# Kernel optimization log

Hardware: AMD Instinct MI355X
Metric: run time of the kernel (lower is better)

The kernel has to match this reference:

```python
import jax, jax.numpy as jnp
import numpy as np

B, C, H, W = 8, 512, 96, 96

def setup_inputs() -> dict:
    key = jax.random.key(0)
    k1, k2, k3, k4, k5 = jax.random.split(key, 5)
    s = 0.02
    return {
        "x": jax.random.normal(k1, (B, C, H, W), dtype=jnp.float32),
        "w_qkv": jax.random.normal(k2, (3 * C, C), dtype=jnp.float32) * s,
        "b_qkv": jax.random.normal(k3, (3 * C,), dtype=jnp.float32) * s,
        "w_proj": jax.random.normal(k4, (C, C), dtype=jnp.float32) * s,
        "b_proj": jax.random.normal(k5, (C,), dtype=jnp.float32) * s,
    }

def reference(x, w_qkv, b_qkv, w_proj, b_proj):
    b, c, h, w = x.shape
    n = h * w
    # 1x1 conv == pointwise linear over channels
    qkv = jnp.einsum('bchw,oc->bohw', x, w_qkv) + b_qkv[None, :, None, None]
    qkv = qkv.reshape(b, 3, c, n)
    q, k, v = qkv[:, 0], qkv[:, 1], qkv[:, 2]  # each [B, C, N]
    # channel attention: scores are [B, C, C]
    scale = 1.0 / (c ** 0.5)
    attn = jax.nn.softmax(jnp.einsum('bcn,bdn->bcd', q, k) * scale, axis=-1)
    out = jnp.einsum('bcd,bdn->bcn', attn, v).reshape(b, c, h, w)
    out = jnp.einsum('bchw,oc->bohw', out, w_proj) + b_proj[None, :, None, None]
    return out
```

## Files before the change

### kernel.cpp

```cpp
#include <hip/hip_runtime.h>

typedef unsigned short u16;
typedef unsigned long long u64;
typedef __bf16 bf16x8 __attribute__((ext_vector_type(8)));
typedef u16 us8 __attribute__((ext_vector_type(8)));
typedef u16 us4 __attribute__((ext_vector_type(4)));
typedef float floatx4 __attribute__((ext_vector_type(4)));
typedef float f32x4 __attribute__((ext_vector_type(4)));

__device__ inline float b2f(u16 u) {
  union { unsigned u; float f; } x; x.u = ((unsigned)u) << 16; return x.f;
}
__device__ inline u16 f2b(float f) {
  union { float f; unsigned u; } x; x.f = f;
  unsigned r = x.u + 0x7fffu + ((x.u >> 16) & 1u);
  return (u16)(r >> 16);
}

__global__ __launch_bounds__(256)
void detect_dtype(const u16* __restrict__ x, int* __restrict__ flag, int force) {
  __shared__ float sm[4];
  const int t = threadIdx.x;
  float m = 0.f;
  for (int i = t; i < 4096; i += 256) {
    float v = fabsf(b2f(x[i]));
    if (v > m) m = v;
  }
#pragma unroll
  for (int o = 32; o; o >>= 1) m = fmaxf(m, __shfl_xor(m, o, 64));
  if ((t & 63) == 0) sm[t >> 6] = m;
  __syncthreads();
  if (t == 0) {
    float mm = fmaxf(fmaxf(sm[0], sm[1]), fmaxf(sm[2], sm[3]));
    *flag = (force >= 0) ? force : (mm > 1000.0f ? 1 : 0);
  }
}

__global__ __launch_bounds__(256)
void convert_bf16(const void* __restrict__ in, u16* __restrict__ out, long n,
                  const int* __restrict__ flag) {
  const long i = (blockIdx.x * 256L + threadIdx.x) * 8;
  if (i >= n) return;
  if (*flag) {
    const float* p = (const float*)in + i;
    f32x4 a = ((const f32x4*)p)[0];
    f32x4 b = ((const f32x4*)p)[1];
    us8 o;
#pragma unroll
    for (int j = 0; j < 4; j++) { o[j] = f2b(a[j]); o[j + 4] = f2b(b[j]); }
    *(us8*)(out + i) = o;
  } else {
    *(us8*)(out + i) = *((const us8*)in + (i >> 3));
  }
}

template <typename OutT>
__global__ __launch_bounds__(256)
void gemm_nt(const u16* __restrict__ A, long sA, int lda,
             const u16* __restrict__ B, long sB, int ldb,
             OutT* __restrict__ D, long sD, int ldd, int K) {
  __shared__ __align__(16) u16 As[128 * 32];
  __shared__ __align__(16) u16 Bs[128 * 32];
  const int bz = blockIdx.z;
  const u16* Ab = A + (long)bz * sA;
  const u16* Bb = B + (long)bz * sB;
  OutT* Db = D + (long)bz * sD;
  const int tid  = threadIdx.x;
  const int lane = tid & 63;
  const int wave = tid >> 6;
  const int wm = (wave >> 1) * 64, wn = (wave & 1) * 64;
  const int m0 = blockIdx.y * 128, n0 = blockIdx.x * 128;
  const int srow = tid >> 2;
  const int ss   = tid & 3;
  const int sw   = (ss ^ ((srow >> 1) & 3)) * 8;
  const int lr = lane & 15;
  const int rsw = (((lane >> 4) ^ ((lr >> 1) & 3)) * 8);

  floatx4 acc[4][4];
#pragma unroll
  for (int i = 0; i < 4; i++)
#pragma unroll
    for (int j = 0; j < 4; j++) acc[i][j] = (floatx4){0.f, 0.f, 0.f, 0.f};

  for (int k0 = 0; k0 < K; k0 += 32) {
    __syncthreads();
    *(bf16x8*)&As[srow * 32 + sw] =
        *(const bf16x8*)&Ab[(long)(m0 + srow) * lda + k0 + ss * 8];
    *(bf16x8*)&As[(srow + 64) * 32 + sw] =
        *(const bf16x8*)&Ab[(long)(m0 + srow + 64) * lda + k0 + ss * 8];
    *(bf16x8*)&Bs[srow * 32 + sw] =
        *(const bf16x8*)&Bb[(long)(n0 + srow) * ldb + k0 + ss * 8];
    *(bf16x8*)&Bs[(srow + 64) * 32 + sw] =
        *(const bf16x8*)&Bb[(long)(n0 + srow + 64) * ldb + k0 + ss * 8];
    __syncthreads();
    bf16x8 af[4], bfr[4];
#pragma unroll
    for (int i = 0; i < 4; i++)
      af[i] = *(bf16x8*)&As[(wm + i * 16 + lr) * 32 + rsw];
#pragma unroll
    for (int i = 0; i < 4; i++)
      bfr[i] = *(bf16x8*)&Bs[(wn + i * 16 + lr) * 32 + rsw];
#pragma unroll
    for (int mi = 0; mi < 4; mi++)
#pragma unroll
      for (int ni = 0; ni < 4; ni++)
        acc[mi][ni] = __builtin_amdgcn_mfma_f32_16x16x32_bf16(
            af[mi], bfr[ni], acc[mi][ni], 0, 0, 0);
  }

  const int lc  = lane & 15;
  const int lr4 = (lane >> 4) * 4;
#pragma unroll
  for (int mi = 0; mi < 4; mi++) {
#pragma unroll
    for (int r = 0; r < 4; r++) {
      int gm = m0 + wm + mi * 16 + lr4 + r;
#pragma unroll
      for (int ni = 0; ni < 4; ni++) {
        int gn = n0 + wn + ni * 16 + lc;
        float v = acc[mi][ni][r];
        if constexpr (sizeof(OutT) == 4) Db[(long)gm * ldd + gn] = v;
        else                             Db[(long)gm * ldd + gn] = f2b(v);
      }
    }
  }
}

__device__ inline void tile_decode(int t, int& by, int& bx) {
  by = (int)((sqrtf((float)(8 * t + 1)) - 1.0f) * 0.5f);
  bx = t - (by * (by + 1)) / 2;
}

__global__ __launch_bounds__(256)
void gemm_xxt_splitk(const u16* __restrict__ X, float* __restrict__ P) {
  __shared__ __align__(16) u16 As[128 * 32];
  __shared__ __align__(16) u16 Bs[128 * 32];
  const int t  = blockIdx.x;
  const int bz = blockIdx.z >> 3;
  const int sp = blockIdx.z & 7;
  int by, bx;
  tile_decode(t, by, bx);
  const int m0 = by * 128, n0 = bx * 128;
  const u16* Xb = X + (long)bz * 512 * 9216;
  const int tid  = threadIdx.x;
  const int lane = tid & 63;
  const int wave = tid >> 6;
  const int wm = (wave >> 1) * 64, wn = (wave & 1) * 64;
  const int srow = tid >> 2;
  const int ss   = tid & 3;
  const int sw   = (ss ^ ((srow >> 1) & 3)) * 8;
  const int lr = lane & 15;
  const int rsw = (((lane >> 4) ^ ((lr >> 1) & 3)) * 8);

  floatx4 acc[4][4];
#pragma unroll
  for (int i = 0; i < 4; i++)
#pragma unroll
    for (int j = 0; j < 4; j++) acc[i][j] = (floatx4){0.f, 0.f, 0.f, 0.f};

  const int k0beg = sp * 1152;
  for (int k0 = k0beg; k0 < k0beg + 1152; k0 += 32) {
    __syncthreads();
    *(bf16x8*)&As[srow * 32 + sw] =
        *(const bf16x8*)&Xb[(long)(m0 + srow) * 9216 + k0 + ss * 8];
    *(bf16x8*)&As[(srow + 64) * 32 + sw] =
        *(const bf16x8*)&Xb[(long)(m0 + srow + 64) * 9216 + k0 + ss * 8];
    *(bf16x8*)&Bs[srow * 32 + sw] =
        *(const bf16x8*)&Xb[(long)(n0 + srow) * 9216 + k0 + ss * 8];
    *(bf16x8*)&Bs[(srow + 64) * 32 + sw] =
        *(const bf16x8*)&Xb[(long)(n0 + srow + 64) * 9216 + k0 + ss * 8];
    __syncthreads();
    bf16x8 af[4], bfr[4];
#pragma unroll
    for (int i = 0; i < 4; i++)
      af[i] = *(bf16x8*)&As[(wm + i * 16 + lr) * 32 + rsw];
#pragma unroll
    for (int i = 0; i < 4; i++)
      bfr[i] = *(bf16x8*)&Bs[(wn + i * 16 + lr) * 32 + rsw];
#pragma unroll
    for (int mi = 0; mi < 4; mi++)
#pragma unroll
      for (int ni = 0; ni < 4; ni++)
        acc[mi][ni] = __builtin_amdgcn_mfma_f32_16x16x32_bf16(
            af[mi], bfr[ni], acc[mi][ni], 0, 0, 0);
  }

  float* Pb = P + ((long)(sp * 8 + bz) * 10 + t) * 16384;
  const int lc  = lane & 15;
  const int lr4 = (lane >> 4) * 4;
#pragma unroll
  for (int mi = 0; mi < 4; mi++)
#pragma unroll
    for (int r = 0; r < 4; r++) {
      int gm = wm + mi * 16 + lr4 + r;
#pragma unroll
      for (int ni = 0; ni < 4; ni++)
        Pb[gm * 128 + wn + ni * 16 + lc] = acc[mi][ni][r];
    }
}

__global__ __launch_bounds__(256)
void reduce_xxt(const float* __restrict__ P, u16* __restrict__ G) {
  __shared__ u16 tl[128][130];
  const int t = blockIdx.x, bz = blockIdx.y;
  int by, bx;
  tile_decode(t, by, bx);
  const int m0 = by * 128, n0 = bx * 128;
  u16* Gb = G + (long)bz * 512 * 512;
  for (int e = threadIdx.x; e < 4096; e += 256) {
    const int idx = e * 4;
    const int m = idx >> 7, n = idx & 127;
    f32x4 s = {0.f, 0.f, 0.f, 0.f};
#pragma unroll
    for (int sp = 0; sp < 8; sp++) {
      f32x4 v = *(const f32x4*)&P[(((long)sp * 8 + bz) * 10 + t) * 16384 + idx];
      s.x += v.x; s.y += v.y; s.z += v.z; s.w += v.w;
    }
    us4 o = {f2b(s.x), f2b(s.y), f2b(s.z), f2b(s.w)};
    *(us4*)&Gb[(long)(m0 + m) * 512 + n0 + n] = o;
    tl[m][n] = o[0]; tl[m][n + 1] = o[1]; tl[m][n + 2] = o[2]; tl[m][n + 3] = o[3];
  }
  if (m0 == n0) return;
  __syncthreads();
  for (int e = threadIdx.x; e < 4096; e += 256) {
    const int idx = e * 4;
    const int nr = idx >> 7, mc = idx & 127;
    us4 o = {tl[mc][nr], tl[mc + 1][nr], tl[mc + 2][nr], tl[mc + 3][nr]};
    *(us4*)&Gb[(long)(n0 + nr) * 512 + m0 + mc] = o;
  }
}

__global__ __launch_bounds__(256)
void gemm_nn_out(const u16* __restrict__ A, const u16* __restrict__ B,
                 const float* __restrict__ bias, void* __restrict__ Dout,
                 const int* __restrict__ flag) {
  __shared__ __align__(16)  u16 As[128 * 32];
  __shared__ __align__(128) u16 Bs[32 * 128];
  const int f = *flag;
  const int bz = blockIdx.z;
  const u16* Ab = A + (long)bz * 512 * 512;
  const u16* Bb = B + (long)bz * 512 * 9216;
  const float* cb = bias + bz * 512;
  const int tid  = threadIdx.x;
  const int lane = tid & 63;
  const int wave = tid >> 6;
  const int wm = (wave >> 1) * 64, wn = (wave & 1) * 64;
  const int m0 = blockIdx.y * 128, n0 = blockIdx.x * 128;
  const int srow = tid >> 2;
  const int ss   = tid & 3;
  const int sw   = (ss ^ ((srow >> 1) & 3)) * 8;
  const int kk  = tid >> 3;
  const int nbw = tid & 7;
  const int lr = lane & 15;
  const int rsw = (((lane >> 4) ^ ((lr >> 1) & 3)) * 8);
  const int stO = (nbw * 8 + (kk >> 2)) * 64 + (kk & 3) * 16;
  const unsigned bsBase = (unsigned)(size_t)(&Bs[0]);
  const unsigned trA = bsBase + (unsigned)((wn >> 4) * 1024 +
                       (lane >> 4) * 256 + (lane & 15) * 8);

  floatx4 acc[4][4];
#pragma unroll
  for (int i = 0; i < 4; i++)
#pragma unroll
    for (int j = 0; j < 4; j++) acc[i][j] = (floatx4){0.f, 0.f, 0.f, 0.f};

  for (int k0 = 0; k0 < 512; k0 += 32) {
    __syncthreads();
    *(bf16x8*)&As[srow * 32 + sw] =
        *(const bf16x8*)&Ab[(long)(m0 + srow) * 512 + k0 + ss * 8];
    *(bf16x8*)&As[(srow + 64) * 32 + sw] =
        *(const bf16x8*)&Ab[(long)(m0 + srow + 64) * 512 + k0 + ss * 8];
    us8 v0 = *(const us8*)&Bb[(long)(k0 + kk) * 9216 + n0 + nbw * 16];
    us8 v1 = *(const us8*)&Bb[(long)(k0 + kk) * 9216 + n0 + nbw * 16 + 8];
    *(us8*)&Bs[stO]     = v0;
    *(us8*)&Bs[stO + 8] = v1;
    __syncthreads();
    bf16x8 af[4];
#pragma unroll
    for (int i = 0; i < 4; i++)
      af[i] = *(bf16x8*)&As[(wm + i * 16 + lr) * 32 + rsw];
    u64 blo[4], bhi[4];
#pragma unroll
    for (int ni = 0; ni < 4; ni++) {
      unsigned a = trA + ni * 1024;
      asm volatile("ds_read_b64_tr_b16 %0, %1" : "=v"(blo[ni]) : "v"(a));
      asm volatile("ds_read_b64_tr_b16 %0, %1 offset:128" : "=v"(bhi[ni]) : "v"(a));
    }
    asm volatile("s_waitcnt lgkmcnt(0)" ::: "memory");
    __builtin_amdgcn_sched_barrier(0);
    bf16x8 bfr[4];
#pragma unroll
    for (int ni = 0; ni < 4; ni++) {
      union { u64 q[2]; bf16x8 v; } u;
      u.q[0] = blo[ni]; u.q[1] = bhi[ni];
      bfr[ni] = u.v;
    }
#pragma unroll
    for (int mi = 0; mi < 4; mi++)
#pragma unroll
      for (int ni = 0; ni < 4; ni++)
        acc[mi][ni] = __builtin_amdgcn_mfma_f32_16x16x32_bf16(
            af[mi], bfr[ni], acc[mi][ni], 0, 0, 0);
  }

  const int lc  = lane & 15;
  const int lr4 = (lane >> 4) * 4;
  if (f) {
    float* Db = (float*)Dout + (long)bz * 512 * 9216;
#pragma unroll
    for (int mi = 0; mi < 4; mi++)
#pragma unroll
      for (int r = 0; r < 4; r++) {
        int gm = m0 + wm + mi * 16 + lr4 + r;
        float bv = cb[gm];
#pragma unroll
        for (int ni = 0; ni < 4; ni++)
          Db[(long)gm * 9216 + n0 + wn + ni * 16 + lc] = acc[mi][ni][r] + bv;
      }
  } else {
    u16* Db = (u16*)Dout + (long)bz * 512 * 9216;
#pragma unroll
    for (int mi = 0; mi < 4; mi++)
#pragma unroll
      for (int r = 0; r < 4; r++) {
        int gm = m0 + wm + mi * 16 + lr4 + r;
        float bv = cb[gm];
#pragma unroll
        for (int ni = 0; ni < 4; ni++)
          Db[(long)gm * 9216 + n0 + wn + ni * 16 + lc] = f2b(acc[mi][ni][r] + bv);
      }
  }
}

__global__ __launch_bounds__(256)
void rowsum(const u16* __restrict__ x, float* __restrict__ r) {
  const int row  = blockIdx.x * 4 + (threadIdx.x >> 6);
  const int lane = threadIdx.x & 63;
  const u16* p = x + (long)row * 9216;
  float s = 0.f;
#pragma unroll
  for (int t = 0; t < 18; t++) {
    us8 v = *(const us8*)&p[t * 512 + lane * 8];
#pragma unroll
    for (int e = 0; e < 8; e++) s += b2f(v[e]);
  }
#pragma unroll
  for (int o = 32; o; o >>= 1) s += __shfl_xor(s, o, 64);
  if (lane == 0) r[row] = s;
}

__global__ __launch_bounds__(256)
void matvec_uw(const u16* __restrict__ w_qkv, const float* __restrict__ r,
               float* __restrict__ u, float* __restrict__ w) {
  const int g = blockIdx.x * 256 + threadIdx.x;
  const int b = g >> 10;
  const int s = (g >> 9) & 1;
  const int i = g & 511;
  const u16* Wrow = w_qkv + (long)(s * 512 + i) * 512;
  const float* rb = r + b * 512;
  float acc = 0.f;
  for (int c = 0; c < 512; c++) acc += b2f(Wrow[c]) * rb[c];
  (s ? w : u)[b * 512 + i] = acc;
}

__global__ __launch_bounds__(256)
void cvec(const u16* __restrict__ w_proj, const float* __restrict__ y,
          const u16* __restrict__ b_proj, float* __restrict__ cv) {
  const int g = blockIdx.x * 256 + threadIdx.x;
  const int b = g >> 9;
  const int o = g & 511;
  const u16* Wrow = w_proj + (long)o * 512;
  const float* yb = y + b * 512;
  float acc = 0.f;
  for (int i = 0; i < 512; i++) acc += b2f(Wrow[i]) * yb[i];
  cv[b * 512 + o] = acc + b2f(b_proj[o]);
}

__global__ __launch_bounds__(256)
void softmax_rank1(const float* __restrict__ Score, const float* __restrict__ u,
                   const float* __restrict__ w, const u16* __restrict__ b_qkv,
                   u16* __restrict__ PT, float* __restrict__ y) {
  const int row  = blockIdx.x * 4 + (threadIdx.x >> 6);
  const int lane = threadIdx.x & 63;
  const int b = row >> 9, i = row & 511;
  const float scale = 0.04419417382415922f;
  const float* srow = Score + (long)row * 512;
  const float* wb = w + b * 512;
  const float bq_i = b2f(b_qkv[i]);
  const float uu = u[row] + 9216.0f * bq_i;
  float vals[8];
  float mx = -1e30f;
#pragma unroll
  for (int t = 0; t < 8; t++) {
    int j = lane + t * 64;
    float s = srow[j] + uu * b2f(b_qkv[512 + j]) + bq_i * wb[j];
    vals[t] = scale * s;
    mx = fmaxf(mx, vals[t]);
  }
#pragma unroll
  for (int o = 32; o; o >>= 1) mx = fmaxf(mx, __shfl_xor(mx, o, 64));
  float sum = 0.f, ys = 0.f;
#pragma unroll
  for (int t = 0; t < 8; t++) {
    int j = lane + t * 64;
    vals[t] = __expf(vals[t] - mx);
    sum += vals[t];
    ys += vals[t] * b2f(b_qkv[1024 + j]);
  }
#pragma unroll
  for (int o = 32; o; o >>= 1) sum += __shfl_xor(sum, o, 64);
#pragma unroll
  for (int o = 32; o; o >>= 1) ys += __shfl_xor(ys, o, 64);
  const float inv = 1.0f / sum;
#pragma unroll
  for (int t = 0; t < 8; t++) {
    int j = lane + t * 64;
    PT[(long)b * 512 * 512 + (long)j * 512 + i] = f2b(vals[t] * inv);
  }
  if (lane == 0) y[row] = ys * inv;
}

__global__ __launch_bounds__(256)
void transpose512(const u16* __restrict__ in, u16* __restrict__ out) {
  __shared__ u16 tile[32][33];
  const int c0 = blockIdx.x * 32, r0 = blockIdx.y * 32;
  const int tx = threadIdx.x, ty = threadIdx.y;
#pragma unroll
  for (int i = 0; i < 32; i += 8)
    tile[ty + i][tx] = in[(long)(r0 + ty + i) * 512 + c0 + tx];
  __syncthreads();
#pragma unroll
  for (int i = 0; i < 32; i += 8)
    out[(long)(c0 + ty + i) * 512 + r0 + tx] = tile[tx][ty + i];
}

extern "C" void kernel_launch(void* const* d_in, const int* in_sizes, int n_in,
                              void* d_out, int out_size, void* d_ws, size_t ws_size,
                              hipStream_t stream) {
  const long CN = 512L * 9216;
  const long SQ = 512L * 512;

  char* ws = (char*)d_ws;
  int*   flag  = (int*)ws;                      ws += 16;
  u16*   Gb    = (u16*)ws;                      ws += 8 * SQ * 2;
  u16*   T1    = (u16*)ws;                      ws += 8 * SQ * 2;
  u16*   PT    = (u16*)ws;                      ws += 8 * SQ * 2;
  u16*   T3    = (u16*)ws;                      ws += 8 * SQ * 2;
  u16*   Mm    = (u16*)ws;                      ws += 8 * SQ * 2;
  float* Score = (float*)ws;                    ws += 8 * SQ * 4;
  u16*   WvT   = (u16*)ws;                      ws += SQ * 2;
  float* r     = (float*)ws;                    ws += 8 * 512 * 4;
  float* u     = (float*)ws;                    ws += 8 * 512 * 4;
  float* w     = (float*)ws;                    ws += 8 * 512 * 4;
  float* y     = (float*)ws;                    ws += 8 * 512 * 4;
  float* cv    = (float*)ws;                    ws += 8 * 512 * 4;
  u16* xc      = (u16*)ws;                      ws += 8 * CN * 2;
  u16* wqkv_c  = (u16*)ws;                      ws += 1536L * 512 * 2;
  u16* bqkv_c  = (u16*)ws;                      ws += 1536L * 2;
  u16* wproj_c = (u16*)ws;                      ws += 512L * 512 * 2;
  u16* bproj_c = (u16*)ws;                      ws += 512L * 2;

  char* mark1 = ws;
  float* Psk  = (float*)ws;                     ws += 8L * 8 * 10 * 16384 * 4;

  const bool full  = ((size_t)(mark1 - (char*)d_ws) <= ws_size);
  const bool full2 = ((size_t)(ws    - (char*)d_ws) <= ws_size);

  if (full) {
    detect_dtype<<<1, 256, 0, stream>>>((const u16*)d_in[0], flag, -1);
    convert_bf16<<<18432, 256, 0, stream>>>(d_in[0], xc,      8 * CN,      flag);
    convert_bf16<<<384,   256, 0, stream>>>(d_in[1], wqkv_c,  1536L * 512, flag);
    convert_bf16<<<1,     256, 0, stream>>>(d_in[2], bqkv_c,  1536,        flag);
    convert_bf16<<<128,   256, 0, stream>>>(d_in[3], wproj_c, 512L * 512,  flag);
    convert_bf16<<<1,     256, 0, stream>>>(d_in[4], bproj_c, 512,         flag);
  } else {
    detect_dtype<<<1, 256, 0, stream>>>((const u16*)d_in[0], flag, 0);
    xc      = (u16*)d_in[0];
    wqkv_c  = (u16*)d_in[1];
    bqkv_c  = (u16*)d_in[2];
    wproj_c = (u16*)d_in[3];
    bproj_c = (u16*)d_in[4];
  }

  const u16* Wq = wqkv_c;
  const u16* Wk = wqkv_c + 512 * 512;
  const u16* Wv = wqkv_c + 1024 * 512;

  if (full2) {
    gemm_xxt_splitk<<<dim3(10, 1, 64), 256, 0, stream>>>(xc, Psk);
    reduce_xxt<<<dim3(10, 8), 256, 0, stream>>>(Psk, Gb);
  } else {
    gemm_nt<u16><<<dim3(4, 4, 8), 256, 0, stream>>>(
        xc, CN, 9216, xc, CN, 9216, Gb, SQ, 512, 9216);
  }
  rowsum<<<1024, 256, 0, stream>>>(xc, r);
  matvec_uw<<<32, 256, 0, stream>>>(wqkv_c, r, u, w);
  gemm_nt<u16><<<dim3(4, 4, 8), 256, 0, stream>>>(
      Wq, 0, 512, Gb, SQ, 512, T1, SQ, 512, 512);
  gemm_nt<float><<<dim3(4, 4, 8), 256, 0, stream>>>(
      T1, SQ, 512, Wk, 0, 512, Score, SQ, 512, 512);
  softmax_rank1<<<1024, 256, 0, stream>>>(Score, u, w, bqkv_c, PT, y);
  transpose512<<<dim3(16, 16), dim3(32, 8), 0, stream>>>(Wv, WvT);
  gemm_nt<u16><<<dim3(4, 4, 8), 256, 0, stream>>>(
      wproj_c, 0, 512, PT, SQ, 512, T3, SQ, 512, 512);
  gemm_nt<u16><<<dim3(4, 4, 8), 256, 0, stream>>>(
      T3, SQ, 512, WvT, 0, 512, Mm, SQ, 512, 512);
  cvec<<<16, 256, 0, stream>>>(wproj_c, y, bproj_c, cv);
  gemm_nn_out<<<dim3(72, 4, 8), 256, 0, stream>>>(Mm, xc, cv, d_out, flag);
}
```

Baseline: 572.6 us.

## Use direct global-to-LDS loads in GEMMs and shrink small GEMM tiles

Replaces register-staged global loads and LDS stores with global_load_lds direct-to-LDS transfers in gemm_nt, the split-K XX^T GEMM and the output GEMM. The per-wave LDS destinations are arranged so the existing swizzle and transposed read pattern still hold. The 512x512 batched GEMMs also drop from 128x128 to 64x64 tiles, launched on an 8x8x8 grid, to put more blocks on the device. This aims to cut VGPR traffic and instruction count for staging and to improve occupancy on the small GEMMs, at the cost of less reuse per tile.

```diff
diff --git a/kernel.cpp b/kernel.cpp
--- a/kernel.cpp
+++ b/kernel.cpp
@@ -15,6 +15,12 @@
   union { float f; unsigned u; } x; x.f = f;
   unsigned r = x.u + 0x7fffu + ((x.u >> 16) & 1u);
   return (u16)(r >> 16);
+}
+
+__device__ __forceinline__ void gl_lds16(const u16* g, void* l) {
+  __builtin_amdgcn_global_load_lds(
+      (const __attribute__((address_space(1))) void*)g,
+      (__attribute__((address_space(3))) void*)l, 16, 0, 0);
 }
 
 __global__ __launch_bounds__(256)
@@ -59,8 +65,8 @@
 void gemm_nt(const u16* __restrict__ A, long sA, int lda,
              const u16* __restrict__ B, long sB, int ldb,
              OutT* __restrict__ D, long sD, int ldd, int K) {
-  __shared__ __align__(16) u16 As[128 * 32];
-  __shared__ __align__(16) u16 Bs[128 * 32];
+  __shared__ __align__(16) u16 As[64 * 32];
+  __shared__ __align__(16) u16 Bs[64 * 32];
   const int bz = blockIdx.z;
   const u16* Ab = A + (long)bz * sA;
   const u16* Bb = B + (long)bz * sB;
@@ -68,42 +74,38 @@
   const int tid  = threadIdx.x;
   const int lane = tid & 63;
   const int wave = tid >> 6;
-  const int wm = (wave >> 1) * 64, wn = (wave & 1) * 64;
-  const int m0 = blockIdx.y * 128, n0 = blockIdx.x * 128;
+  const int wm = (wave >> 1) * 32, wn = (wave & 1) * 32;
+  const int m0 = blockIdx.y * 64, n0 = blockIdx.x * 64;
   const int srow = tid >> 2;
   const int ss   = tid & 3;
-  const int sw   = (ss ^ ((srow >> 1) & 3)) * 8;
+  const int sco  = (ss ^ ((srow >> 1) & 3)) * 8;
   const int lr = lane & 15;
   const int rsw = (((lane >> 4) ^ ((lr >> 1) & 3)) * 8);
-
-  floatx4 acc[4][4];
-#pragma unroll
-  for (int i = 0; i < 4; i++)
-#pragma unroll
-    for (int j = 0; j < 4; j++) acc[i][j] = (floatx4){0.f, 0.f, 0.f, 0.f};
+  char* asb = (char*)As + wave * 1024;
+  char* bsb = (char*)Bs + wave * 1024;
+
+  floatx4 acc[2][2];
+#pragma unroll
+  for (int i = 0; i < 2; i++)
+#pragma unroll
+    for (int j = 0; j < 2; j++) acc[i][j] = (floatx4){0.f, 0.f, 0.f, 0.f};
 
   for (int k0 = 0; k0 < K; k0 += 32) {
     __syncthreads();
-    *(bf16x8*)&As[srow * 32 + sw] =
-        *(const bf16x8*)&Ab[(long)(m0 + srow) * lda + k0 + ss * 8];
-    *(bf16x8*)&As[(srow + 64) * 32 + sw] =
-        *(const bf16x8*)&Ab[(long)(m0 + srow + 64) * lda + k0 + ss * 8];
-    *(bf16x8*)&Bs[srow * 32 + sw] =
-        *(const bf16x8*)&Bb[(long)(n0 + srow) * ldb + k0 + ss * 8];
-    *(bf16x8*)&Bs[(srow + 64) * 32 + sw] =
-        *(const bf16x8*)&Bb[(long)(n0 + srow + 64) * ldb + k0 + ss * 8];
+    gl_lds16(&Ab[(long)(m0 + srow) * lda + k0 + sco], asb);
+    gl_lds16(&Bb[(long)(n0 + srow) * ldb + k0 + sco], bsb);
     __syncthreads();
-    bf16x8 af[4], bfr[4];
-#pragma unroll
-    for (int i = 0; i < 4; i++)
+    bf16x8 af[2], bfr[2];
+#pragma unroll
+    for (int i = 0; i < 2; i++)
       af[i] = *(bf16x8*)&As[(wm + i * 16 + lr) * 32 + rsw];
 #pragma unroll
-    for (int i = 0; i < 4; i++)
+    for (int i = 0; i < 2; i++)
       bfr[i] = *(bf16x8*)&Bs[(wn + i * 16 + lr) * 32 + rsw];
 #pragma unroll
-    for (int mi = 0; mi < 4; mi++)
-#pragma unroll
-      for (int ni = 0; ni < 4; ni++)
+    for (int mi = 0; mi < 2; mi++)
+#pragma unroll
+      for (int ni = 0; ni < 2; ni++)
         acc[mi][ni] = __builtin_amdgcn_mfma_f32_16x16x32_bf16(
             af[mi], bfr[ni], acc[mi][ni], 0, 0, 0);
   }
@@ -111,12 +113,12 @@
   const int lc  = lane & 15;
   const int lr4 = (lane >> 4) * 4;
 #pragma unroll
-  for (int mi = 0; mi < 4; mi++) {
+  for (int mi = 0; mi < 2; mi++) {
 #pragma unroll
     for (int r = 0; r < 4; r++) {
       int gm = m0 + wm + mi * 16 + lr4 + r;
 #pragma unroll
-      for (int ni = 0; ni < 4; ni++) {
+      for (int ni = 0; ni < 2; ni++) {
         int gn = n0 + wn + ni * 16 + lc;
         float v = acc[mi][ni][r];
         if constexpr (sizeof(OutT) == 4) Db[(long)gm * ldd + gn] = v;
@@ -148,9 +150,11 @@
   const int wm = (wave >> 1) * 64, wn = (wave & 1) * 64;
   const int srow = tid >> 2;
   const int ss   = tid & 3;
-  const int sw   = (ss ^ ((srow >> 1) & 3)) * 8;
+  const int sco  = (ss ^ ((srow >> 1) & 3)) * 8;
   const int lr = lane & 15;
   const int rsw = (((lane >> 4) ^ ((lr >> 1) & 3)) * 8);
+  char* asb = (char*)As + wave * 1024;
+  char* bsb = (char*)Bs + wave * 1024;
 
   floatx4 acc[4][4];
 #pragma unroll
@@ -161,14 +165,10 @@
   const int k0beg = sp * 1152;
   for (int k0 = k0beg; k0 < k0beg + 1152; k0 += 32) {
     __syncthreads();
-    *(bf16x8*)&As[srow * 32 + sw] =
-        *(const bf16x8*)&Xb[(long)(m0 + srow) * 9216 + k0 + ss * 8];
-    *(bf16x8*)&As[(srow + 64) * 32 + sw] =
-        *(const bf16x8*)&Xb[(long)(m0 + srow + 64) * 9216 + k0 + ss * 8];
-    *(bf16x8*)&Bs[srow * 32 + sw] =
-        *(const bf16x8*)&Xb[(long)(n0 + srow) * 9216 + k0 + ss * 8];
-    *(bf16x8*)&Bs[(srow + 64) * 32 + sw] =
-        *(const bf16x8*)&Xb[(long)(n0 + srow + 64) * 9216 + k0 + ss * 8];
+    gl_lds16(&Xb[(long)(m0 + srow) * 9216 + k0 + sco], asb);
+    gl_lds16(&Xb[(long)(m0 + 64 + srow) * 9216 + k0 + sco], asb + 4096);
+    gl_lds16(&Xb[(long)(n0 + srow) * 9216 + k0 + sco], bsb);
+    gl_lds16(&Xb[(long)(n0 + 64 + srow) * 9216 + k0 + sco], bsb + 4096);
     __syncthreads();
     bf16x8 af[4], bfr[4];
 #pragma unroll
@@ -248,12 +248,13 @@
   const int m0 = blockIdx.y * 128, n0 = blockIdx.x * 128;
   const int srow = tid >> 2;
   const int ss   = tid & 3;
-  const int sw   = (ss ^ ((srow >> 1) & 3)) * 8;
-  const int kk  = tid >> 3;
-  const int nbw = tid & 7;
+  const int sco  = (ss ^ ((srow >> 1) & 3)) * 8;
   const int lr = lane & 15;
   const int rsw = (((lane >> 4) ^ ((lr >> 1) & 3)) * 8);
-  const int stO = (nbw * 8 + (kk >> 2)) * 64 + (kk & 3) * 16;
+  char* asb = (char*)As + wave * 1024;
+  char* bsb = (char*)Bs + wave * 1024;
+  const int bs_k = ((tid >> 3) & 7) * 4 + ((tid >> 1) & 3);
+  const int bs_n = (tid >> 6) * 16 + (tid & 1) * 8;
   const unsigned bsBase = (unsigned)(size_t)(&Bs[0]);
   const unsigned trA = bsBase + (unsigned)((wn >> 4) * 1024 +
                        (lane >> 4) * 256 + (lane & 15) * 8);
@@ -266,14 +267,11 @@
 
   for (int k0 = 0; k0 < 512; k0 += 32) {
     __syncthreads();
-    *(bf16x8*)&As[srow * 32 + sw] =
-        *(const bf16x8*)&Ab[(long)(m0 + srow) * 512 + k0 + ss * 8];
-    *(bf16x8*)&As[(srow + 64) * 32 + sw] =
-        *(const bf16x8*)&Ab[(long)(m0 + srow + 64) * 512 + k0 + ss * 8];
-    us8 v0 = *(const us8*)&Bb[(long)(k0 + kk) * 9216 + n0 + nbw * 16];
-    us8 v1 = *(const us8*)&Bb[(long)(k0 + kk) * 9216 + n0 + nbw * 16 + 8];
-    *(us8*)&Bs[stO]     = v0;
-    *(us8*)&Bs[stO + 8] = v1;
+    gl_lds16(&Ab[(long)(m0 + srow) * 512 + k0 + sco], asb);
+    gl_lds16(&Ab[(long)(m0 + 64 + srow) * 512 + k0 + sco], asb + 4096);
+    const u16* bp = &Bb[(long)(k0 + bs_k) * 9216 + n0 + bs_n];
+    gl_lds16(bp, bsb);
+    gl_lds16(bp + 64, bsb + 4096);
     __syncthreads();
     bf16x8 af[4];
 #pragma unroll
@@ -490,20 +488,20 @@
     gemm_xxt_splitk<<<dim3(10, 1, 64), 256, 0, stream>>>(xc, Psk);
     reduce_xxt<<<dim3(10, 8), 256, 0, stream>>>(Psk, Gb);
   } else {
-    gemm_nt<u16><<<dim3(4, 4, 8), 256, 0, stream>>>(
+    gemm_nt<u16><<<dim3(8, 8, 8), 256, 0, stream>>>(
         xc, CN, 9216, xc, CN, 9216, Gb, SQ, 512, 9216);
   }
   rowsum<<<1024, 256, 0, stream>>>(xc, r);
   matvec_uw<<<32, 256, 0, stream>>>(wqkv_c, r, u, w);
-  gemm_nt<u16><<<dim3(4, 4, 8), 256, 0, stream>>>(
+  gemm_nt<u16><<<dim3(8, 8, 8), 256, 0, stream>>>(
       Wq, 0, 512, Gb, SQ, 512, T1, SQ, 512, 512);
-  gemm_nt<float><<<dim3(4, 4, 8), 256, 0, stream>>>(
+  gemm_nt<float><<<dim3(8, 8, 8), 256, 0, stream>>>(
       T1, SQ, 512, Wk, 0, 512, Score, SQ, 512, 512);
   softmax_rank1<<<1024, 256, 0, stream>>>(Score, u, w, bqkv_c, PT, y);
   transpose512<<<dim3(16, 16), dim3(32, 8), 0, stream>>>(Wv, WvT);
-  gemm_nt<u16><<<dim3(4, 4, 8), 256, 0, stream>>>(
+  gemm_nt<u16><<<dim3(8, 8, 8), 256, 0, stream>>>(
       wproj_c, 0, 512, PT, SQ, 512, T3, SQ, 512, 512);
-  gemm_nt<u16><<<dim3(4, 4, 8), 256, 0, stream>>>(
+  gemm_nt<u16><<<dim3(8, 8, 8), 256, 0, stream>>>(
       T3, SQ, 512, WvT, 0, 512, Mm, SQ, 512, 512);
   cvec<<<16, 256, 0, stream>>>(wproj_c, y, bproj_c, cv);
   gemm_nn_out<<<dim3(72, 4, 8), 256, 0, stream>>>(Mm, xc, cv, d_out, flag);
```

Measured after the change: 550.4 us. 3.9% less time.
